# Optimization experiments

Hardware: AMD Instinct MI355X
Metric: run time of the kernel (lower is better)

The kernel has to match this reference:

```python
import jax, jax.numpy as jnp
import numpy as np

B, S, DIN, H, Q = 64, 1024, 256, 512, 64


def setup_inputs() -> dict:
    key = jax.random.key(0)
    ks = jax.random.split(key, 16)
    def w(k, shape, scale=0.02):
        return jax.random.normal(k, shape, jnp.float32) * scale
    return {
        "seq_input": jax.random.normal(ks[0], (B, S, DIN), jnp.float32),
        "quality_input": jax.random.normal(ks[1], (B, S, Q), jnp.float32),
        "mask": jax.random.randint(ks[2], (B, S), 0, 2, jnp.int32),
        "ln_g": jnp.ones((DIN,), jnp.float32),
        "ln_b": jnp.zeros((DIN,), jnp.float32),
        "Wp": w(ks[3], (DIN, H)), "bp": jnp.zeros((H,), jnp.float32),
        "Wc": w(ks[4], (H, 1, 3)), "bc": jnp.zeros((H,), jnp.float32),  # depthwise conv (OIH)
        "Wq": w(ks[5], (Q, H)), "bq": jnp.zeros((H,), jnp.float32),
        "Wmw": w(ks[6], (2 * H, H)), "bmw": jnp.zeros((H,), jnp.float32),
        "Wmc": w(ks[7], (3 * H, H)), "bmc": jnp.zeros((H,), jnp.float32),
        "Wow": w(ks[8], (2 * H, H)), "bow": jnp.zeros((H,), jnp.float32),
        "Woc": w(ks[9], (3 * H, H)), "boc": jnp.zeros((H,), jnp.float32),
        "Wrw": w(ks[10], (2 * H, H)), "brw": jnp.zeros((H,), jnp.float32),
        "Wrc": w(ks[11], (3 * H, H)), "brc": jnp.zeros((H,), jnp.float32),
        "Wo": w(ks[12], (3 * H, H)), "bo": jnp.zeros((H,), jnp.float32),
    }


def reference(seq_input, quality_input, mask, ln_g, ln_b, Wp, bp, Wc, bc, Wq, bq,
              Wmw, bmw, Wmc, bmc, Wow, bow, Woc, boc, Wrw, brw, Wrc, brc, Wo, bo):
    h = Wp.shape[1]
    # LayerNorm (eps=1e-5)
    mu = jnp.mean(seq_input, axis=-1, keepdims=True)
    var = jnp.mean(jnp.square(seq_input - mu), axis=-1, keepdims=True)
    xn = (seq_input - mu) / jnp.sqrt(var + 1e-5) * ln_g + ln_b
    # input projection + depthwise local mixer (kernel 3, pad 1)
    hid = xn @ Wp + bp  # (B,S,H)
    hid = jax.lax.conv_general_dilated(
        hid.transpose(0, 2, 1), Wc, window_strides=(1,), padding=((1, 1),),
        feature_group_count=h, dimension_numbers=("NCH", "OIH", "NCH"),
    ).transpose(0, 2, 1) + bc  # (B,S,H)
    qe = quality_input @ Wq + bq  # (B,S,H)

    xs = hid.transpose(1, 0, 2)              # (S,B,H)
    qs = qe.transpose(1, 0, 2)               # (S,B,H)
    vs = (mask > 0).T[..., None]             # (S,B,1) bool

    def step(carry, inp):
        m, o, r = carry
        x, q, v = inp
        mw = jax.nn.sigmoid(jnp.concatenate([x, q], -1) @ Wmw + bmw)
        mc = jnp.tanh(jnp.concatenate([x, q, o], -1) @ Wmc + bmc)
        ow = jax.nn.sigmoid(jnp.concatenate([q, m], -1) @ Wow + bow)
        oc = jnp.tanh(jnp.concatenate([q, m, r], -1) @ Woc + boc)
        rw = jax.nn.sigmoid(jnp.concatenate([q, o], -1) @ Wrw + brw)
        rc = jnp.tanh(jnp.concatenate([x, m, o], -1) @ Wrc + brc)
        nm = jnp.where(v, (1.0 - mw) * m + mw * mc, m)
        no = jnp.where(v, (1.0 - ow) * o + ow * oc, o)
        nr = jnp.where(v, (1.0 - rw) * r + rw * rc, r)
        out = jnp.concatenate([nm, no, nr], -1) @ Wo + bo
        return (nm, no, nr), out

    z = jnp.zeros((hid.shape[0], h), hid.dtype)
    (m, o, r), outs = jax.lax.scan(step, (z, z, z), (xs, qs, vs))
    outputs = outs.transpose(1, 0, 2) + hid  # dropout is identity in eval mode
    return (outputs, m, o, r)
```

## Files before the change

### kernel.cpp

```cpp
#include <hip/hip_runtime.h>
#include <hip/hip_bf16.h>
#include <cstdint>
#include <cstddef>

#define DEV static __device__ __forceinline__

typedef unsigned short u16;
typedef __attribute__((ext_vector_type(8))) short short8;
typedef __attribute__((ext_vector_type(4))) short short4v;
typedef __attribute__((ext_vector_type(4))) float f32x4;
typedef __attribute__((ext_vector_type(4))) int i32x4;

constexpr int B = 64, S = 1024, DIN = 256, H = 512;
constexpr int BS = B * S;

DEV float b2f(u16 u) { union { unsigned int i; float f; } v; v.i = ((unsigned int)u) << 16; return v.f; }
DEV u16 f2u(float f) {
  __hip_bfloat16 h = __float2bfloat16(f);
  u16 r; __builtin_memcpy(&r, &h, 2); return r;
}
DEV float sigf(float x) { return 1.0f / (1.0f + __expf(-x)); }
DEV float ldf(const void* p, size_t i, int isf) {
  return isf ? ((const float*)p)[i] : b2f(((const u16*)p)[i]);
}

DEV void gload_lds16(const void* g, void* l) {
  __builtin_amdgcn_global_load_lds(
      (const __attribute__((address_space(1))) unsigned int*)g,
      (__attribute__((address_space(3))) unsigned int*)l, 16, 0, 0);
}

DEV i32x4 cload16(const void* g) {
  i32x4 v;
  asm volatile("global_load_dwordx4 %0, %1, off sc0 sc1" : "=v"(v) : "v"(g));
  return v;
}

__global__ void detect_kernel(const u16* __restrict__ g, int* __restrict__ flag) {
  if (threadIdx.x == 0) flag[0] = (g[0] == (u16)0) ? 1 : 0;
}

__global__ __launch_bounds__(256) void ln_kernel(const void* __restrict__ x,
    const void* __restrict__ gw, const void* __restrict__ bw, u16* __restrict__ xn,
    const int* __restrict__ dfl) {
  int isf = dfl[0];
  int tid = threadIdx.x, lane = tid & 63, wid = tid >> 6;
  size_t t = (size_t)blockIdx.x * 4 + wid;
  float f[4];
  if (isf) {
    f32x4 v = *(const f32x4*)((const float*)x + t * DIN + lane * 4);
#pragma unroll
    for (int j = 0; j < 4; j++) f[j] = v[j];
  } else {
    short4v v = *(const short4v*)((const u16*)x + t * DIN + lane * 4);
#pragma unroll
    for (int j = 0; j < 4; j++) f[j] = b2f((u16)v[j]);
  }
  float s0 = f[0] + f[1] + f[2] + f[3];
  float s1 = f[0]*f[0] + f[1]*f[1] + f[2]*f[2] + f[3]*f[3];
#pragma unroll
  for (int off = 32; off; off >>= 1) { s0 += __shfl_xor(s0, off); s1 += __shfl_xor(s1, off); }
  float mu = s0 * (1.0f / DIN);
  float var = s1 * (1.0f / DIN) - mu * mu;
  float rs = rsqrtf(var + 1e-5f);
  short4v o;
#pragma unroll
  for (int j = 0; j < 4; j++) {
    float xv = (f[j] - mu) * rs * ldf(gw, lane*4 + j, isf) + ldf(bw, lane*4 + j, isf);
    o[j] = (short)f2u(xv);
  }
  *(short4v*)(xn + t * DIN + lane * 4) = o;
}

__global__ void transpose_kernel(const void* __restrict__ in, u16* __restrict__ out,
                                 int R, int C, const int* __restrict__ dfl) {
  int isf = dfl[0];
  int idx = blockIdx.x * 256 + threadIdx.x;
  if (idx >= R * C) return;
  int r = idx / C, c = idx - r * C;
  out[(size_t)c * R + r] = isf ? f2u(((const float*)in)[idx]) : ((const u16*)in)[idx];
}

__global__ __launch_bounds__(256) void cast_kernel(const void* __restrict__ in,
    u16* __restrict__ out, int n, const int* __restrict__ dfl) {
  int isf = dfl[0];
  int i0 = (blockIdx.x * 256 + threadIdx.x) * 8;
  if (i0 >= n) return;
  short8 o;
  if (isf) {
    f32x4 a = *(const f32x4*)((const float*)in + i0);
    f32x4 b = *(const f32x4*)((const float*)in + i0 + 4);
#pragma unroll
    for (int j = 0; j < 4; j++) { o[j] = (short)f2u(a[j]); o[j+4] = (short)f2u(b[j]); }
  } else {
    o = *(const short8*)((const u16*)in + i0);
  }
  *(short8*)(out + i0) = o;
}

__global__ __launch_bounds__(256) void conv_kernel(const u16* __restrict__ h0,
    const void* __restrict__ Wc, const void* __restrict__ bc, u16* __restrict__ hid,
    const int* __restrict__ dfl) {
  int isf = dfl[0];
  int tid = threadIdx.x;
  size_t token = (size_t)blockIdx.x * 4 + (tid >> 6);
  int lane = tid & 63;
  int s = (int)(token & (size_t)(S - 1));
  int hh = lane * 8;
  const u16* pm = h0 + token * H + hh;
  short8 vm = *(const short8*)pm;
  short8 vp = {0,0,0,0,0,0,0,0}, vn = {0,0,0,0,0,0,0,0};
  if (s > 0) vp = *(const short8*)(pm - H);
  if (s < S - 1) vn = *(const short8*)(pm + H);
  float w[24];
#pragma unroll
  for (int j = 0; j < 24; j++) w[j] = ldf(Wc, (size_t)hh * 3 + j, isf);
  short8 vo;
#pragma unroll
  for (int i = 0; i < 8; i++) {
    float acc = ldf(bc, hh + i, isf);
    acc += b2f((u16)vp[i]) * w[i*3 + 0];
    acc += b2f((u16)vm[i]) * w[i*3 + 1];
    acc += b2f((u16)vn[i]) * w[i*3 + 2];
    vo[i] = (short)f2u(acc);
  }
  *(short8*)(hid + token * H + hh) = vo;
}

DEV int swz(int row, int kbyte) { return row * 128 + (kbyte ^ ((row & 7) << 4)); }

__global__ __launch_bounds__(256) void gemm_kernel(
    const u16* __restrict__ A, const u16* __restrict__ Bt,
    const void* __restrict__ bias, const u16* __restrict__ res,
    void* __restrict__ C, int K, const int* __restrict__ dfl, int out_ds) {
  int isf = dfl[0];
  __shared__ __align__(16) char sA[128 * 64 * 2];
  __shared__ __align__(16) char sB[128 * 64 * 2];
  int tid = threadIdx.x, lane = tid & 63, wid = tid >> 6;
  int wr = wid >> 1, wc = wid & 1;
  int m0 = blockIdx.y * 128, n0 = blockIdx.x * 128;
  f32x4 zf = {0.f, 0.f, 0.f, 0.f};
  f32x4 acc[4][4];
#pragma unroll
  for (int a = 0; a < 4; a++)
#pragma unroll
    for (int b = 0; b < 4; b++) acc[a][b] = zf;
  int nsteps = K >> 6;
  for (int kt = 0; kt < nsteps; kt++) {
    int k0 = kt << 6;
    __syncthreads();
#pragma unroll
    for (int ri = 0; ri < 4; ri++) {
      int ci = ri * 256 + tid;
      int row = ci >> 3, kc = ci & 7;
      *(short8*)(sA + swz(row, kc * 16)) = *(const short8*)(A + (size_t)(m0 + row) * K + k0 + kc * 8);
      *(short8*)(sB + swz(row, kc * 16)) = *(const short8*)(Bt + (size_t)(n0 + row) * K + k0 + kc * 8);
    }
    __syncthreads();
#pragma unroll
    for (int kk = 0; kk < 2; kk++) {
      int kb = (kk * 32 + ((lane >> 4) * 8)) * 2;
      short8 af[4], bf[4];
#pragma unroll
      for (int t = 0; t < 4; t++) af[t] = *(const short8*)(sA + swz(wr * 64 + t * 16 + (lane & 15), kb));
#pragma unroll
      for (int t = 0; t < 4; t++) bf[t] = *(const short8*)(sB + swz(wc * 64 + t * 16 + (lane & 15), kb));
#pragma unroll
      for (int tr = 0; tr < 4; tr++)
#pragma unroll
        for (int tc = 0; tc < 4; tc++)
          acc[tr][tc] = __builtin_amdgcn_mfma_f32_16x16x32_bf16(af[tr], bf[tc], acc[tr][tc], 0, 0, 0);
    }
  }
#pragma unroll
  for (int tr = 0; tr < 4; tr++) {
#pragma unroll
    for (int tc = 0; tc < 4; tc++) {
      int n = n0 + wc * 64 + tc * 16 + (lane & 15);
      float bv = ldf(bias, n, isf);
#pragma unroll
      for (int jj = 0; jj < 4; jj++) {
        int m = m0 + wr * 64 + tr * 16 + ((lane >> 4) * 4) + jj;
        size_t idx = (size_t)m * 512 + n;
        float v = acc[tr][tc][jj] + bv;
        if (res) v += b2f(res[idx]);
        if (out_ds && isf) ((float*)C)[idx] = v;
        else ((u16*)C)[idx] = f2u(v);
      }
    }
  }
}

__global__ __launch_bounds__(256, 1) void seq_kernel(
    const u16* __restrict__ hid, const u16* __restrict__ qe, const int* __restrict__ mask,
    const void* __restrict__ Wmw, const void* __restrict__ bmw,
    const void* __restrict__ Wmc, const void* __restrict__ bmc,
    const void* __restrict__ Wow, const void* __restrict__ bow,
    const void* __restrict__ Woc, const void* __restrict__ boc,
    const void* __restrict__ Wrw, const void* __restrict__ brw,
    const void* __restrict__ Wrc, const void* __restrict__ brc,
    u16* __restrict__ hist, void* __restrict__ dout, unsigned int* __restrict__ ctr,
    const int* __restrict__ dfl) {

  constexpr int PITCHA = (1024 + 8) * 2;
  constexpr int PITCHB = (1536 + 8) * 2;
  constexpr int RED_OFF = 49408;
  constexpr int ST_OFF = RED_OFF + 12288;
  constexpr int BIAS_OFF = ST_OFF + 1536;
  constexpr int MASK_OFF = BIAS_OFF + 192;
  constexpr int DEAD_OFF = MASK_OFF + 64;
  __shared__ __align__(16) char lds_raw[DEAD_OFF + 16];

  float* REDf = (float*)(lds_raw + RED_OFF);
  float* STf = (float*)(lds_raw + ST_OFF);
  float* BIASf = (float*)(lds_raw + BIAS_OFF);
  int* MASKi = (int*)(lds_raw + MASK_OFF);
  int* DEADi = (int*)(lds_raw + DEAD_OFF);

  int isf = dfl[0];
  int tid = threadIdx.x, lane = tid & 63, wid = tid >> 6;
  int g = blockIdx.x >> 6, cb = blockIdx.x & 63;
  int b0 = g * 16, c0 = cb * 8;

  constexpr int NTS[5] = {3, 3, 3, 2, 1};
  constexpr int FBASE[5] = {0, 12, 24, 36, 44};
  constexpr int TLIST[5][3] = { {0,1,2}, {0,1,2}, {0,1,2}, {1,2,0}, {1,0,0} };
  constexpr int WSEL[3][5][2] = {
    { {0,-1}, {0,2}, {-1,2}, {-1,-1}, {-1,-1} },
    { {1,-1}, {1,3}, {-1,3}, {1,-1}, {-1,3} },
    { {-1,5}, {4,-1}, {-1,5}, {4,5}, {-1,-1} },
  };
  constexpr int ROFF[3][5][2] = {
    { {0,0}, {512,0}, {0,512}, {0,0}, {0,0} },
    { {0,0}, {512,0}, {0,512}, {1024,0}, {0,1024} },
    { {0,0}, {0,0}, {0,512}, {512,1024}, {0,0} },
  };

  short8 wfrag[48];
  {
    int col16 = lane & 15, half = col16 >> 3;
    int coln = c0 + (col16 & 7);
#pragma unroll
    for (int sec = 0; sec < 5; sec++) {
#pragma unroll
      for (int j = 0; j < 4; j++) {
#pragma unroll
        for (int ti = 0; ti < 3; ti++) {
          if (ti >= NTS[sec]) continue;
          const int tile = TLIST[sec][ti];
          int wsel = WSEL[tile][sec][half];
          int ro = ROFF[tile][sec][half];
          const void* wp = (wsel == 0) ? Wmw : (wsel == 1) ? Wmc : (wsel == 2) ? Wow
                         : (wsel == 3) ? Woc : (wsel == 4) ? Wrw : Wrc;
          short8 f8;
#pragma unroll
          for (int jj = 0; jj < 8; jj++) {
            int kin = (j * 4 + wid) * 32 + ((lane >> 4) * 8) + jj;
            u16 v = 0;
            if (wsel >= 0) v = f2u(ldf(wp, (size_t)(ro + kin) * 512 + coln, isf));
            f8[jj] = (short)v;
          }
          wfrag[FBASE[sec] + j * NTS[sec] + ti] = f8;
        }
      }
    }
  }
  if (tid < 48) {
    int gate = tid >> 3, col = tid & 7;
    const void* bp_ = (gate == 0) ? bmw : (gate == 1) ? bmc : (gate == 2) ? bow
                    : (gate == 3) ? boc : (gate == 4) ? brw : brc;
    BIASf[tid] = ldf(bp_, c0 + col, isf);
  }
  if (tid < 128) { STf[tid*3] = 0.f; STf[tid*3+1] = 0.f; STf[tid*3+2] = 0.f; }
  if (tid == 0) DEADi[0] = 0;
  __syncthreads();

  bool dead = false;
  for (int s = 0; s < S; s++) {
    {
      int r0 = wid * 4;
#pragma unroll
      for (int rr = 0; rr < 4; rr++) {
        int b = b0 + r0 + rr;
        const u16* gx = hid + ((size_t)b * S + s) * H;
        const u16* gq = qe + ((size_t)b * S + s) * H;
        char* lx = lds_raw + (size_t)(r0 + rr) * PITCHA;
        gload_lds16(gx + lane * 8, lx);
        gload_lds16(gq + lane * 8, lx + 1024);
      }
    }
    if (tid < 16) MASKi[tid] = mask[(size_t)(b0 + tid) * S + s];
    asm volatile("s_waitcnt vmcnt(0)" ::: "memory");
    __syncthreads();

    f32x4 zf = {0.f, 0.f, 0.f, 0.f};
    f32x4 acc[3]; acc[0] = zf; acc[1] = zf; acc[2] = zf;

#pragma unroll
    for (int sec = 0; sec < 2; sec++) {
#pragma unroll
      for (int j = 0; j < 4; j++) {
        const short8 a = *(const short8*)(lds_raw + (size_t)(lane & 15) * PITCHA + sec * 1024 +
                                          ((j * 4 + wid) * 32 + ((lane >> 4) * 8)) * 2);
#pragma unroll
        for (int ti = 0; ti < 3; ti++) {
          if (ti >= NTS[sec]) continue;
          const int tile = TLIST[sec][ti];
          acc[tile] = __builtin_amdgcn_mfma_f32_16x16x32_bf16(a, wfrag[FBASE[sec] + j * NTS[sec] + ti], acc[tile], 0, 0, 0);
        }
      }
    }

    if (tid == 0 && s > 0 && !dead) {
      unsigned int it = 0;
      while (__hip_atomic_load(&ctr[g * S + s - 1], __ATOMIC_RELAXED, __HIP_MEMORY_SCOPE_AGENT) < 64u) {
        if (++it > (1u << 22)) { dead = true; DEADi[0] = 1; break; }
      }
    }
    __syncthreads();

    if (s == 0) {
      short8 z8 = {0,0,0,0,0,0,0,0};
#pragma unroll
      for (int rr = 0; rr < 4; rr++) {
        char* lr = lds_raw + (size_t)(wid * 4 + rr) * PITCHB;
#pragma unroll
        for (int sc = 0; sc < 3; sc++)
          *(short8*)(lr + sc * 1024 + lane * 16) = z8;
      }
    } else {
      i32x4 v[12];
#pragma unroll
      for (int rr = 0; rr < 4; rr++) {
        int b = b0 + wid * 4 + rr;
        const char* gm = (const char*)(hist + ((size_t)b * S + (s - 1)) * 1536);
#pragma unroll
        for (int sc = 0; sc < 3; sc++)
          v[rr * 3 + sc] = cload16(gm + sc * 1024 + lane * 16);
      }
      asm volatile("s_waitcnt vmcnt(0)" ::: "memory");
#pragma unroll
      for (int rr = 0; rr < 4; rr++) {
        char* lr = lds_raw + (size_t)(wid * 4 + rr) * PITCHB;
#pragma unroll
        for (int sc = 0; sc < 3; sc++)
          *(i32x4*)(lr + sc * 1024 + lane * 16) = v[rr * 3 + sc];
      }
    }
    __syncthreads();

#pragma unroll
    for (int sec = 2; sec < 5; sec++) {
#pragma unroll
      for (int j = 0; j < 4; j++) {
        const short8 a = *(const short8*)(lds_raw + (size_t)(lane & 15) * PITCHB + (sec - 2) * 1024 +
                                          ((j * 4 + wid) * 32 + ((lane >> 4) * 8)) * 2);
#pragma unroll
        for (int ti = 0; ti < 3; ti++) {
          if (ti >= NTS[sec]) continue;
          const int tile = TLIST[sec][ti];
          acc[tile] = __builtin_amdgcn_mfma_f32_16x16x32_bf16(a, wfrag[FBASE[sec] + j * NTS[sec] + ti], acc[tile], 0, 0, 0);
        }
      }
    }
#pragma unroll
    for (int t = 0; t < 3; t++)
      *(f32x4*)(REDf + (wid * 3 + t) * 256 + lane * 4) = acc[t];
    __syncthreads();

    if (tid < 128) {
      int row = tid >> 3, col = tid & 7;
      int lbase = ((row >> 2) * 16) * 4 + (row & 3);
      auto rd = [&](int tile, int col16) {
        int e = lbase + col16 * 4;
        return REDf[(0 * 3 + tile) * 256 + e] + REDf[(1 * 3 + tile) * 256 + e] +
               REDf[(2 * 3 + tile) * 256 + e] + REDf[(3 * 3 + tile) * 256 + e];
      };
      float pmw = rd(0, col)     + BIASf[0 * 8 + col];
      float pmc = rd(1, col)     + BIASf[1 * 8 + col];
      float pow_ = rd(0, col + 8) + BIASf[2 * 8 + col];
      float poc = rd(1, col + 8) + BIASf[3 * 8 + col];
      float prw = rd(2, col)     + BIASf[4 * 8 + col];
      float prc = rd(2, col + 8) + BIASf[5 * 8 + col];
      float mwv = sigf(pmw), mcv = tanhf(pmc);
      float owv = sigf(pow_), ocv = tanhf(poc);
      float rwv = sigf(prw), rcv = tanhf(prc);
      float* st = STf + (row * 8 + col) * 3;
      float m_ = st[0], o_ = st[1], r_ = st[2];
      bool v = MASKi[row] > 0;
      float nm = v ? (1.f - mwv) * m_ + mwv * mcv : m_;
      float no = v ? (1.f - owv) * o_ + owv * ocv : o_;
      float nr = v ? (1.f - rwv) * r_ + rwv * rcv : r_;
      if (DEADi[0]) { nm = 12345.0f; no = 12345.0f; nr = 12345.0f; }
      st[0] = nm; st[1] = no; st[2] = nr;
      size_t hb = ((size_t)(b0 + row) * S + s) * 1536 + c0 + col;
      __hip_atomic_store(&hist[hb], f2u(nm), __ATOMIC_RELAXED, __HIP_MEMORY_SCOPE_SYSTEM);
      __hip_atomic_store(&hist[hb + 512], f2u(no), __ATOMIC_RELAXED, __HIP_MEMORY_SCOPE_SYSTEM);
      __hip_atomic_store(&hist[hb + 1024], f2u(nr), __ATOMIC_RELAXED, __HIP_MEMORY_SCOPE_SYSTEM);
    }
    __syncthreads();
    if (tid == 0)
      __hip_atomic_fetch_add(&ctr[g * S + s], 1u, __ATOMIC_RELAXED, __HIP_MEMORY_SCOPE_AGENT);
  }

  if (tid < 128) {
    int row = tid >> 3, col = tid & 7;
    float* st = STf + (row * 8 + col) * 3;
    size_t bi = (size_t)(b0 + row) * H + c0 + col;
    size_t obase = (size_t)BS * 512;
    size_t BH = (size_t)B * H;
    if (isf) {
      float* p = (float*)dout;
      p[obase + bi] = st[0]; p[obase + BH + bi] = st[1]; p[obase + 2*BH + bi] = st[2];
    } else {
      u16* p = (u16*)dout;
      p[obase + bi] = f2u(st[0]); p[obase + BH + bi] = f2u(st[1]); p[obase + 2*BH + bi] = f2u(st[2]);
    }
  }
}

extern "C" void kernel_launch(void* const* d_in, const int* in_sizes, int n_in,
                              void* d_out, int out_size, void* d_ws, size_t ws_size,
                              hipStream_t stream) {
  (void)in_sizes; (void)n_in;
  const void* seq = d_in[0];
  const void* qual = d_in[1];
  const int* mask = (const int*)d_in[2];
  const void* ln_g = d_in[3];
  const void* ln_b = d_in[4];
  const void* Wp = d_in[5];
  const void* bp = d_in[6];
  const void* Wc = d_in[7];
  const void* bc = d_in[8];
  const void* Wq = d_in[9];
  const void* bq = d_in[10];
  const void* Wmw = d_in[11];
  const void* bmw = d_in[12];
  const void* Wmc = d_in[13];
  const void* bmc = d_in[14];
  const void* Wow = d_in[15];
  const void* bow = d_in[16];
  const void* Woc = d_in[17];
  const void* boc = d_in[18];
  const void* Wrw = d_in[19];
  const void* brw = d_in[20];
  const void* Wrc = d_in[21];
  const void* brc = d_in[22];
  const void* Wo = d_in[23];
  const void* bo = d_in[24];

  char* wsb = (char*)d_ws;
  size_t off = 0;
  u16* hist = (u16*)(wsb + off); off += (size_t)BS * 1536 * 2;
  u16* hid = (u16*)(wsb + off); off += (size_t)BS * 512 * 2;
  u16* qe = (u16*)(wsb + off); off += (size_t)BS * 512 * 2;
  u16* WpT = (u16*)(wsb + off); off += (size_t)512 * 256 * 2;
  u16* WqT = (u16*)(wsb + off); off += (size_t)512 * 64 * 2;
  u16* WoT = (u16*)(wsb + off); off += (size_t)512 * 1536 * 2;
  unsigned int* ctr = (unsigned int*)(wsb + off); off += 4 * 1024 * 4;
  int* dflag = (int*)(wsb + off); off += 64;
  if (ws_size < off) {
    hipMemsetAsync(d_out, 0x42, (size_t)out_size * 2, stream);
    return;
  }

  u16* xn = hist;
  u16* hid0 = hist + (size_t)BS * 256;
  u16* qual_bf = hist + (size_t)BS * 768;

  hipMemsetAsync(ctr, 0, 4 * 1024 * 4, stream);

  detect_kernel<<<1, 64, 0, stream>>>((const u16*)ln_g, dflag);

  ln_kernel<<<BS / 4, 256, 0, stream>>>(seq, ln_g, ln_b, xn, dflag);
  transpose_kernel<<<(256 * 512 + 255) / 256, 256, 0, stream>>>(Wp, WpT, 256, 512, dflag);
  transpose_kernel<<<(64 * 512 + 255) / 256, 256, 0, stream>>>(Wq, WqT, 64, 512, dflag);
  transpose_kernel<<<(1536 * 512 + 255) / 256, 256, 0, stream>>>(Wo, WoT, 1536, 512, dflag);
  cast_kernel<<<(BS * 64 / 8 + 255) / 256, 256, 0, stream>>>(qual, qual_bf, BS * 64, dflag);

  gemm_kernel<<<dim3(4, BS / 128), 256, 0, stream>>>(xn, WpT, bp, nullptr, hid0, 256, dflag, 0);
  conv_kernel<<<BS / 4, 256, 0, stream>>>(hid0, Wc, bc, hid, dflag);
  gemm_kernel<<<dim3(4, BS / 128), 256, 0, stream>>>(qual_bf, WqT, bq, nullptr, qe, 64, dflag, 0);

  seq_kernel<<<256, 256, 0, stream>>>(hid, qe, mask,
      Wmw, bmw, Wmc, bmc, Wow, bow, Woc, boc, Wrw, brw, Wrc, brc,
      hist, d_out, ctr, dflag);

  gemm_kernel<<<dim3(4, BS / 128), 256, 0, stream>>>(hist, WoT, bo, hid, d_out, 1536, dflag, 1);
}
```

Measured before the change: 4.362 ms.

## Prefetch next-step inputs into registers, shard step counters, use fast gate math

Loads the next timestep's hid/qe rows and mask into registers while the current step computes, then writes them to LDS after the reduction. This takes the global load latency off the serial per-step critical path. The single per-group step counter is split into 8 counters that a whole wavefront polls in parallel, which is meant to reduce atomic contention among the 64 blocks. Sigmoid and tanh now use rcp/exp approximations, trading a little accuracy for fewer instructions.

```diff
diff --git a/kernel.cpp b/kernel.cpp
--- a/kernel.cpp
+++ b/kernel.cpp
@@ -19,20 +19,20 @@
   __hip_bfloat16 h = __float2bfloat16(f);
   u16 r; __builtin_memcpy(&r, &h, 2); return r;
 }
-DEV float sigf(float x) { return 1.0f / (1.0f + __expf(-x)); }
+DEV float sigf(float x) { return __builtin_amdgcn_rcpf(1.0f + __expf(-x)); }
+DEV float tanhfast(float x) { return 1.0f - 2.0f * __builtin_amdgcn_rcpf(1.0f + __expf(2.0f * x)); }
 DEV float ldf(const void* p, size_t i, int isf) {
   return isf ? ((const float*)p)[i] : b2f(((const u16*)p)[i]);
-}
-
-DEV void gload_lds16(const void* g, void* l) {
-  __builtin_amdgcn_global_load_lds(
-      (const __attribute__((address_space(1))) unsigned int*)g,
-      (__attribute__((address_space(3))) unsigned int*)l, 16, 0, 0);
 }
 
 DEV i32x4 cload16(const void* g) {
   i32x4 v;
   asm volatile("global_load_dwordx4 %0, %1, off sc0 sc1" : "=v"(v) : "v"(g));
+  return v;
+}
+DEV i32x4 nload16(const void* g) {
+  i32x4 v;
+  asm volatile("global_load_dwordx4 %0, %1, off" : "=v"(v) : "v"(g));
   return v;
 }
 
@@ -199,7 +199,7 @@
     const void* __restrict__ Woc, const void* __restrict__ boc,
     const void* __restrict__ Wrw, const void* __restrict__ brw,
     const void* __restrict__ Wrc, const void* __restrict__ brc,
-    u16* __restrict__ hist, void* __restrict__ dout, unsigned int* __restrict__ ctr,
+    u16* __restrict__ hist, void* __restrict__ dout, unsigned int* __restrict__ ctr2,
     const int* __restrict__ dfl) {
 
   constexpr int PITCHA = (1024 + 8) * 2;
@@ -221,6 +221,7 @@
   int tid = threadIdx.x, lane = tid & 63, wid = tid >> 6;
   int g = blockIdx.x >> 6, cb = blockIdx.x & 63;
   int b0 = g * 16, c0 = cb * 8;
+  int r0 = wid * 4;
 
   constexpr int NTS[5] = {3, 3, 3, 2, 1};
   constexpr int FBASE[5] = {0, 12, 24, 36, 44};
@@ -273,29 +274,38 @@
   }
   if (tid < 128) { STf[tid*3] = 0.f; STf[tid*3+1] = 0.f; STf[tid*3+2] = 0.f; }
   if (tid == 0) DEADi[0] = 0;
+
+  i32x4 px[4], pq[4];
+  int mreg_cur = 0, mreg_next = 0;
+#pragma unroll
+  for (int rr = 0; rr < 4; rr++) {
+    int b = b0 + r0 + rr;
+    px[rr] = nload16(hid + ((size_t)b * S) * H + lane * 8);
+    pq[rr] = nload16(qe + ((size_t)b * S) * H + lane * 8);
+  }
+  if (tid < 16) mreg_cur = mask[(size_t)(b0 + tid) * S];
+  asm volatile("s_waitcnt vmcnt(0)" ::: "memory");
+#pragma unroll
+  for (int rr = 0; rr < 4; rr++) {
+    char* lx = lds_raw + (size_t)(r0 + rr) * PITCHA;
+    *(i32x4*)(lx + lane * 16) = px[rr];
+    *(i32x4*)(lx + 1024 + lane * 16) = pq[rr];
+  }
   __syncthreads();
 
   bool dead = false;
   for (int s = 0; s < S; s++) {
-    {
-      int r0 = wid * 4;
-#pragma unroll
-      for (int rr = 0; rr < 4; rr++) {
-        int b = b0 + r0 + rr;
-        const u16* gx = hid + ((size_t)b * S + s) * H;
-        const u16* gq = qe + ((size_t)b * S + s) * H;
-        char* lx = lds_raw + (size_t)(r0 + rr) * PITCHA;
-        gload_lds16(gx + lane * 8, lx);
-        gload_lds16(gq + lane * 8, lx + 1024);
-      }
-    }
-    if (tid < 16) MASKi[tid] = mask[(size_t)(b0 + tid) * S + s];
-    asm volatile("s_waitcnt vmcnt(0)" ::: "memory");
-    __syncthreads();
+    int sn = (s + 1 < S) ? s + 1 : s;
+#pragma unroll
+    for (int rr = 0; rr < 4; rr++) {
+      int b = b0 + r0 + rr;
+      px[rr] = nload16(hid + ((size_t)b * S + sn) * H + lane * 8);
+      pq[rr] = nload16(qe + ((size_t)b * S + sn) * H + lane * 8);
+    }
+    if (tid < 16) mreg_next = mask[(size_t)(b0 + tid) * S + sn];
 
     f32x4 zf = {0.f, 0.f, 0.f, 0.f};
     f32x4 acc[3]; acc[0] = zf; acc[1] = zf; acc[2] = zf;
-
 #pragma unroll
     for (int sec = 0; sec < 2; sec++) {
 #pragma unroll
@@ -311,10 +321,15 @@
       }
     }
 
-    if (tid == 0 && s > 0 && !dead) {
+    if (s > 0 && wid == 0 && !dead) {
+      const unsigned int* fp = ctr2 + (((size_t)g * S + (s - 1)) << 3);
       unsigned int it = 0;
-      while (__hip_atomic_load(&ctr[g * S + s - 1], __ATOMIC_RELAXED, __HIP_MEMORY_SCOPE_AGENT) < 64u) {
-        if (++it > (1u << 22)) { dead = true; DEADi[0] = 1; break; }
+      for (;;) {
+        unsigned int v = 8u;
+        if (lane < 8)
+          v = __hip_atomic_load(fp + lane, __ATOMIC_RELAXED, __HIP_MEMORY_SCOPE_AGENT);
+        if (__all(v == 8u)) break;
+        if (++it > (1u << 22)) { dead = true; if (lane == 0) DEADi[0] = 1; break; }
       }
     }
     __syncthreads();
@@ -323,7 +338,7 @@
       short8 z8 = {0,0,0,0,0,0,0,0};
 #pragma unroll
       for (int rr = 0; rr < 4; rr++) {
-        char* lr = lds_raw + (size_t)(wid * 4 + rr) * PITCHB;
+        char* lr = lds_raw + (size_t)(r0 + rr) * PITCHB;
 #pragma unroll
         for (int sc = 0; sc < 3; sc++)
           *(short8*)(lr + sc * 1024 + lane * 16) = z8;
@@ -332,7 +347,7 @@
       i32x4 v[12];
 #pragma unroll
       for (int rr = 0; rr < 4; rr++) {
-        int b = b0 + wid * 4 + rr;
+        int b = b0 + r0 + rr;
         const char* gm = (const char*)(hist + ((size_t)b * S + (s - 1)) * 1536);
 #pragma unroll
         for (int sc = 0; sc < 3; sc++)
@@ -341,12 +356,13 @@
       asm volatile("s_waitcnt vmcnt(0)" ::: "memory");
 #pragma unroll
       for (int rr = 0; rr < 4; rr++) {
-        char* lr = lds_raw + (size_t)(wid * 4 + rr) * PITCHB;
+        char* lr = lds_raw + (size_t)(r0 + rr) * PITCHB;
 #pragma unroll
         for (int sc = 0; sc < 3; sc++)
           *(i32x4*)(lr + sc * 1024 + lane * 16) = v[rr * 3 + sc];
       }
     }
+    if (tid < 16) MASKi[tid] = mreg_cur;
     __syncthreads();
 
 #pragma unroll
@@ -367,6 +383,15 @@
     for (int t = 0; t < 3; t++)
       *(f32x4*)(REDf + (wid * 3 + t) * 256 + lane * 4) = acc[t];
     __syncthreads();
+
+    asm volatile("s_waitcnt vmcnt(0)" ::: "memory");
+#pragma unroll
+    for (int rr = 0; rr < 4; rr++) {
+      char* lx = lds_raw + (size_t)(r0 + rr) * PITCHA;
+      *(i32x4*)(lx + lane * 16) = px[rr];
+      *(i32x4*)(lx + 1024 + lane * 16) = pq[rr];
+    }
+    mreg_cur = mreg_next;
 
     if (tid < 128) {
       int row = tid >> 3, col = tid & 7;
@@ -382,9 +407,9 @@
       float poc = rd(1, col + 8) + BIASf[3 * 8 + col];
       float prw = rd(2, col)     + BIASf[4 * 8 + col];
       float prc = rd(2, col + 8) + BIASf[5 * 8 + col];
-      float mwv = sigf(pmw), mcv = tanhf(pmc);
-      float owv = sigf(pow_), ocv = tanhf(poc);
-      float rwv = sigf(prw), rcv = tanhf(prc);
+      float mwv = sigf(pmw), mcv = tanhfast(pmc);
+      float owv = sigf(pow_), ocv = tanhfast(poc);
+      float rwv = sigf(prw), rcv = tanhfast(prc);
       float* st = STf + (row * 8 + col) * 3;
       float m_ = st[0], o_ = st[1], r_ = st[2];
       bool v = MASKi[row] > 0;
@@ -400,7 +425,8 @@
     }
     __syncthreads();
     if (tid == 0)
-      __hip_atomic_fetch_add(&ctr[g * S + s], 1u, __ATOMIC_RELAXED, __HIP_MEMORY_SCOPE_AGENT);
+      __hip_atomic_fetch_add(&ctr2[(((size_t)g * S + s) << 3) | (cb & 7)], 1u,
+                             __ATOMIC_RELAXED, __HIP_MEMORY_SCOPE_AGENT);
   }
 
   if (tid < 128) {
@@ -457,7 +483,7 @@
   u16* WpT = (u16*)(wsb + off); off += (size_t)512 * 256 * 2;
   u16* WqT = (u16*)(wsb + off); off += (size_t)512 * 64 * 2;
   u16* WoT = (u16*)(wsb + off); off += (size_t)512 * 1536 * 2;
-  unsigned int* ctr = (unsigned int*)(wsb + off); off += 4 * 1024 * 4;
+  unsigned int* ctr2 = (unsigned int*)(wsb + off); off += (size_t)4 * 1024 * 8 * 4;
   int* dflag = (int*)(wsb + off); off += 64;
   if (ws_size < off) {
     hipMemsetAsync(d_out, 0x42, (size_t)out_size * 2, stream);
@@ -468,7 +494,7 @@
   u16* hid0 = hist + (size_t)BS * 256;
   u16* qual_bf = hist + (size_t)BS * 768;
 
-  hipMemsetAsync(ctr, 0, 4 * 1024 * 4, stream);
+  hipMemsetAsync(ctr2, 0, (size_t)4 * 1024 * 8 * 4, stream);
 
   detect_kernel<<<1, 64, 0, stream>>>((const u16*)ln_g, dflag);
 
@@ -484,7 +510,7 @@
 
   seq_kernel<<<256, 256, 0, stream>>>(hid, qe, mask,
       Wmw, bmw, Wmc, bmc, Wow, bow, Woc, boc, Wrw, brw, Wrc, brc,
-      hist, d_out, ctr, dflag);
+      hist, d_out, ctr2, dflag);
 
   gemm_kernel<<<dim3(4, BS / 128), 256, 0, stream>>>(hist, WoT, bo, hid, d_out, 1536, dflag, 1);
 }
```

Result: slower. 4.818 ms (+10.4%).
